# Performance work log

Hardware: AMD Instinct MI355X
Metric: run time of the kernel (lower is better)

The kernel has to match this reference:

```python
import jax, jax.numpy as jnp
import numpy as np

D_MODEL = 2048
N_Q = 32
N_KV = 8
HEAD_DIM = D_MODEL // N_Q  # 64
N_REP = N_Q // N_KV        # 4
QKV_OUT = HEAD_DIM * (N_Q + 2 * N_KV)  # 3072


def setup_inputs() -> dict:
    key = jax.random.key(0)
    ks = jax.random.split(key, 6)
    s = 1.0 / np.sqrt(D_MODEL)
    x = jax.random.normal(ks[0], (2, 2048, D_MODEL), dtype=jnp.float32)
    Wqkv = jax.random.normal(ks[1], (D_MODEL, QKV_OUT), dtype=jnp.float32) * s
    bqkv = jax.random.normal(ks[2], (QKV_OUT,), dtype=jnp.float32) * 0.02
    Wo = jax.random.normal(ks[3], (D_MODEL, D_MODEL), dtype=jnp.float32) * s
    bo = jax.random.normal(ks[4], (D_MODEL,), dtype=jnp.float32) * 0.02
    return {"x": x, "Wqkv": Wqkv, "bqkv": bqkv, "Wo": Wo, "bo": bo}


def reference(x, Wqkv, bqkv, Wo, bo):
    bsz, seqlen, _ = x.shape
    qkv = jnp.einsum('bsd,df->bsf', x, Wqkv) + bqkv
    q_end = HEAD_DIM * N_Q
    k_end = q_end + HEAD_DIM * N_KV
    q = qkv[..., :q_end].reshape(bsz, seqlen, N_Q, HEAD_DIM)
    k = qkv[..., q_end:k_end].reshape(bsz, seqlen, N_KV, HEAD_DIM)
    v = qkv[..., k_end:].reshape(bsz, seqlen, N_KV, HEAD_DIM)
    # GQA expansion: repeat kv heads n_rep times -> [b, s, N_Q, hd]
    k = jnp.repeat(k, N_REP, axis=2)
    v = jnp.repeat(v, N_REP, axis=2)
    # scores [b, h, s, s]
    scores = jnp.einsum('bqhd,bkhd->bhqk', q, k) / np.sqrt(HEAD_DIM).astype(np.float32)
    attn = jax.nn.softmax(scores, axis=-1)
    out = jnp.einsum('bhqk,bkhd->bqhd', attn, v).reshape(bsz, seqlen, D_MODEL)
    return jnp.einsum('bsd,de->bse', out, Wo) + bo
```

## Files before the change

kernel.cpp:

```cpp
#include <hip/hip_runtime.h>
#include <stdint.h>

typedef __attribute__((ext_vector_type(8))) __bf16 bf16x8;
typedef __attribute__((ext_vector_type(4))) float f32x4;
typedef uint16_t u16;
typedef __attribute__((address_space(1))) uint32_t ga_u32;
typedef __attribute__((address_space(3))) uint32_t lds_u32;

#define MFMA16(a, b, c) __builtin_amdgcn_mfma_f32_16x16x32_bf16(a, b, c, 0, 0, 0)

static __device__ __forceinline__ u16 f2bf(float f) {
  uint32_t u = __float_as_uint(f);
  u += 0x7FFFu + ((u >> 16) & 1u);
  return (u16)(u >> 16);
}

static __device__ __forceinline__ void async_cp16(const void* src, void* dst) {
  __builtin_amdgcn_global_load_lds((ga_u32*)src, (lds_u32*)dst, 16, 0, 0);
}

__global__ void cast_bf16_kernel(const float* __restrict__ in, u16* __restrict__ out, int n4) {
  int i = blockIdx.x * 256 + threadIdx.x;
  if (i < n4) {
    float4 v = reinterpret_cast<const float4*>(in)[i];
    ushort4 o;
    o.x = f2bf(v.x); o.y = f2bf(v.y); o.z = f2bf(v.z); o.w = f2bf(v.w);
    reinterpret_cast<ushort4*>(out)[i] = o;
  }
}

__global__ void transpose_cast_kernel(const float* __restrict__ W, u16* __restrict__ WT,
                                      int K, int N) {
  __shared__ float tile[32][33];
  int tx = threadIdx.x & 31, ty = threadIdx.x >> 5;
  int n0 = blockIdx.x * 32, k0 = blockIdx.y * 32;
#pragma unroll
  for (int i = 0; i < 32; i += 8)
    tile[ty + i][tx] = W[(size_t)(k0 + ty + i) * N + n0 + tx];
  __syncthreads();
#pragma unroll
  for (int i = 0; i < 32; i += 8)
    WT[(size_t)(n0 + ty + i) * K + k0 + tx] = f2bf(tile[tx][ty + i]);
}

template <int MODE>
__global__ void gemm_bt_kernel(const u16* __restrict__ A, const u16* __restrict__ BT,
                               const float* __restrict__ bias, void* __restrict__ C,
                               u16* __restrict__ vT,
                               int NBX, int N, int K, int OUTN) {
  __shared__ __align__(16) u16 sA[2][128 * 32];
  __shared__ __align__(16) u16 sB[2][128 * 32];
  int tid = threadIdx.x, lane = tid & 63, wave = tid >> 6;
  int wm = wave >> 1, wn = wave & 1;
  int nwg = gridDim.x, wid = blockIdx.x;
  int swz = (wid & 7) * (nwg >> 3) + (wid >> 3);
  int by = swz / NBX, bx = swz - by * NBX;
  int row0 = by * 128, col0 = bx * 128;
  int l15 = lane & 15, l4 = lane >> 4;

  int srow = wave * 32 + (lane >> 2);
  int sslot = (((lane & 3) ^ ((srow >> 1) & 3))) * 8;
  auto stage = [&](const u16* g, int r0, int k0, u16* lds) {
#pragma unroll
    for (int j = 0; j < 2; ++j) {
      const u16* src = g + (size_t)(r0 + srow + j * 16) * K + k0 + sslot;
      async_cp16(src, lds + (wave * 2 + j) * 512);
    }
  };

  f32x4 acc[4][4] = {};
  stage(A, row0, 0, sA[0]);
  stage(BT, col0, 0, sB[0]);
  __syncthreads();
  int nk = K >> 5, cur = 0;
  for (int kt = 0; kt < nk; ++kt) {
    if (kt + 1 < nk) {
      stage(A, row0, (kt + 1) * 32, sA[cur ^ 1]);
      stage(BT, col0, (kt + 1) * 32, sB[cur ^ 1]);
    }
    bf16x8 af[4], bfr[4];
#pragma unroll
    for (int m = 0; m < 4; ++m) {
      int ra = wm * 64 + m * 16 + l15;
      af[m] = *reinterpret_cast<const bf16x8*>(&sA[cur][ra * 32 + ((l4 ^ ((ra >> 1) & 3)) & 3) * 8]);
    }
#pragma unroll
    for (int n = 0; n < 4; ++n) {
      int rb = wn * 64 + n * 16 + l15;
      bfr[n] = *reinterpret_cast<const bf16x8*>(&sB[cur][rb * 32 + ((l4 ^ ((rb >> 1) & 3)) & 3) * 8]);
    }
#pragma unroll
    for (int m = 0; m < 4; ++m)
#pragma unroll
      for (int n = 0; n < 4; ++n)
        acc[m][n] = MFMA16(af[m], bfr[n], acc[m][n]);
    __syncthreads();
    cur ^= 1;
  }

  bool vpart = (MODE == 1) && (col0 >= 2560);
#pragma unroll
  for (int m = 0; m < 4; ++m) {
#pragma unroll
    for (int n = 0; n < 4; ++n) {
      int col = col0 + wn * 64 + n * 16 + l15;
      float bv = bias[col];
      int rowb = row0 + wm * 64 + m * 16 + l4 * 4;
      if (vpart) {
        int hk = (col - 2560) >> 6, d = col & 63;
        int b = rowb >> 11, s = rowb & 2047;
        ushort4 o;
        o.x = f2bf(acc[m][n][0] + bv); o.y = f2bf(acc[m][n][1] + bv);
        o.z = f2bf(acc[m][n][2] + bv); o.w = f2bf(acc[m][n][3] + bv);
        *reinterpret_cast<ushort4*>(&vT[((size_t)((b * 8 + hk) * 64 + d)) * 2048 + s]) = o;
      } else {
#pragma unroll
        for (int e = 0; e < 4; ++e) {
          float v = acc[m][n][e] + bv;
          if (MODE == 1)
            ((u16*)C)[(size_t)(rowb + e) * OUTN + col] = f2bf(v);
          else
            ((float*)C)[(size_t)(rowb + e) * OUTN + col] = v;
        }
      }
    }
  }
}

__global__ __launch_bounds__(256, 4)
void attn_kernel(const u16* __restrict__ qkv, const u16* __restrict__ vTg,
                 u16* __restrict__ attno) {
  __shared__ __align__(16) u16 Kl[2][64 * 64];
  __shared__ __align__(16) u16 Vl[2][64 * 64];
  __shared__ __align__(16) u16 Pw[4][1024];

  int wid = blockIdx.x;
  int swz = (wid & 7) * 128 + (wid >> 3);
  int qt = swz & 15, bh = swz >> 4;
  int b = bh >> 5, h = bh & 31, g = h >> 2;
  int tid = threadIdx.x, lane = tid & 63, w = tid >> 6;
  int l15 = lane & 15, l4 = lane >> 4;
  size_t rowbase = (size_t)b * 2048;

  bf16x8 aq[2][2];
#pragma unroll
  for (int qf = 0; qf < 2; ++qf)
#pragma unroll
    for (int ks = 0; ks < 2; ++ks)
      aq[qf][ks] = *reinterpret_cast<const bf16x8*>(
          qkv + (rowbase + qt * 128 + w * 32 + qf * 16 + l15) * 2560 + h * 64 + ks * 32 + l4 * 8);

  int src_r = lane >> 3;
  int sslot = ((lane & 7) ^ src_r) * 8;
  const u16* Kg = qkv + rowbase * 2560 + 2048 + g * 64;
  const u16* Vg = vTg + ((size_t)((b * 8 + g) * 64)) * 2048;

  auto stageKV = [&](int kt, int buf) {
#pragma unroll
    for (int j = 0; j < 2; ++j) {
      int c = w * 2 + j;
      async_cp16(Kg + (size_t)(kt * 64 + c * 8 + src_r) * 2560 + sslot, &Kl[buf][c * 512]);
    }
#pragma unroll
    for (int j = 0; j < 2; ++j) {
      int c = w * 2 + j;
      async_cp16(Vg + (size_t)(c * 8 + src_r) * 2048 + kt * 64 + sslot, &Vl[buf][c * 512]);
    }
  };

  f32x4 oacc[2][4] = {};
  f32x4 lacc[2] = {};
  union { short s[8]; bf16x8 v; } ones;
#pragma unroll
  for (int i = 0; i < 8; ++i) ones.s[i] = 0x3F80;

  stageKV(0, 0);
  const float CEXP = 0.18033688011112042f;
  char* pwb = (char*)&Pw[w][0];

  for (int kt = 0; kt < 32; ++kt) {
    int cur = kt & 1;
    __syncthreads();
    if (kt + 1 < 32) stageKV(kt + 1, cur ^ 1);

    f32x4 s[2][4] = {};
#pragma unroll
    for (int ks = 0; ks < 2; ++ks) {
      bf16x8 bk[4];
#pragma unroll
      for (int kf = 0; kf < 4; ++kf) {
        int key = kf * 16 + l15;
        bk[kf] = *reinterpret_cast<const bf16x8*>(
            &Kl[cur][key * 64 + (((ks * 4 + l4) ^ (key & 7)) * 8)]);
      }
#pragma unroll
      for (int qf = 0; qf < 2; ++qf)
#pragma unroll
        for (int kf = 0; kf < 4; ++kf)
          s[qf][kf] = MFMA16(bk[kf], aq[qf][ks], s[qf][kf]);
    }

#pragma unroll
    for (int qf = 0; qf < 2; ++qf)
#pragma unroll
      for (int kf = 0; kf < 4; ++kf)
#pragma unroll
        for (int e = 0; e < 4; ++e)
          s[qf][kf][e] = __builtin_amdgcn_exp2f(s[qf][kf][e] * CEXP);

#pragma unroll
    for (int kc = 0; kc < 2; ++kc) {
#pragma unroll
      for (int qf = 0; qf < 2; ++qf) {
        int ql = qf * 16 + l15;
#pragma unroll
        for (int kh = 0; kh < 2; ++kh) {
          union { ushort4 u; __bf16 bb[4]; } pk;
#pragma unroll
          for (int e = 0; e < 4; ++e) pk.bb[e] = (__bf16)s[qf][kc * 2 + kh][e];
          int off = ((ql << 6) + (kh << 5) + (l4 << 3)) ^ ((ql & 3) << 4);
          *reinterpret_cast<ushort4*>(pwb + off) = pk.u;
        }
      }
      asm volatile("" ::: "memory");
      bf16x8 pa[2], bv[4];
#pragma unroll
      for (int qf = 0; qf < 2; ++qf) {
        int ql = qf * 16 + l15;
        int off = ((ql << 6) + (l4 << 4)) ^ ((ql & 3) << 4);
        pa[qf] = *reinterpret_cast<const bf16x8*>(pwb + off);
      }
#pragma unroll
      for (int df = 0; df < 4; ++df) {
        int d = df * 16 + l15;
        bv[df] = *reinterpret_cast<const bf16x8*>(
            &Vl[cur][d * 64 + (((kc * 4 + l4) ^ (d & 7)) * 8)]);
      }
#pragma unroll
      for (int qf = 0; qf < 2; ++qf) {
        lacc[qf] = MFMA16(pa[qf], ones.v, lacc[qf]);
#pragma unroll
        for (int df = 0; df < 4; ++df)
          oacc[qf][df] = MFMA16(pa[qf], bv[df], oacc[qf][df]);
      }
      asm volatile("" ::: "memory");
    }
  }

#pragma unroll
  for (int qf = 0; qf < 2; ++qf)
#pragma unroll
    for (int df = 0; df < 4; ++df) {
      int col = h * 64 + df * 16 + l15;
#pragma unroll
      for (int e = 0; e < 4; ++e) {
        size_t row = rowbase + qt * 128 + w * 32 + qf * 16 + l4 * 4 + e;
        attno[row * 2048 + col] = f2bf(oacc[qf][df][e] / lacc[qf][e]);
      }
    }
}

extern "C" void kernel_launch(void* const* d_in, const int* in_sizes, int n_in,
                              void* d_out, int out_size, void* d_ws, size_t ws_size,
                              hipStream_t stream) {
  const float* x    = (const float*)d_in[0];
  const float* Wqkv = (const float*)d_in[1];
  const float* bqkv = (const float*)d_in[2];
  const float* Wo   = (const float*)d_in[3];
  const float* bo   = (const float*)d_in[4];
  float* out = (float*)d_out;

  char* ws = (char*)d_ws;
  u16* x_bf   = (u16*)(ws);
  u16* WqkvT  = (u16*)(ws + 16777216);
  u16* WoT    = (u16*)(ws + 29360128);
  u16* qkv_bf = (u16*)(ws + 37748736);
  u16* attno  = (u16*)(ws + 58720256);
  u16* vT     = (u16*)(ws + 75497472);

  cast_bf16_kernel<<<8192, 256, 0, stream>>>(x, x_bf, 2097152);
  transpose_cast_kernel<<<dim3(96, 64), 256, 0, stream>>>(Wqkv, WqkvT, 2048, 3072);
  transpose_cast_kernel<<<dim3(64, 64), 256, 0, stream>>>(Wo, WoT, 2048, 2048);
  gemm_bt_kernel<1><<<768, 256, 0, stream>>>(x_bf, WqkvT, bqkv, qkv_bf, vT,
                                             24, 3072, 2048, 2560);
  attn_kernel<<<1024, 256, 0, stream>>>(qkv_bf, vT, attno);
  gemm_bt_kernel<0><<<512, 256, 0, stream>>>(attno, WoT, bo, out, nullptr,
                                             16, 2048, 2048, 2048);
}
```

Measured before the change: 314.9 us.

## Enlarge GEMM and attention tiles to raise K/V and B-tile reuse

The GEMM kernel now runs 512 threads per block with a 256x128 tile, so eight waves share each staged B tile and the grid halves. The attention kernel gives each wave 64 query rows instead of 32, reusing each staged K/V tile across twice as many queries. It also computes the full 64-key score block per query fragment before the PV pass, with a larger per-wave P buffer and a wider XOR swizzle. The trade is more registers and LDS per block, lower occupancy (launch bounds lowered to 2), and fewer blocks to fill the GPU.

```diff
diff --git a/kernel.cpp b/kernel.cpp
--- a/kernel.cpp
+++ b/kernel.cpp
@@ -44,40 +44,40 @@
 }
 
 template <int MODE>
-__global__ void gemm_bt_kernel(const u16* __restrict__ A, const u16* __restrict__ BT,
-                               const float* __restrict__ bias, void* __restrict__ C,
-                               u16* __restrict__ vT,
-                               int NBX, int N, int K, int OUTN) {
-  __shared__ __align__(16) u16 sA[2][128 * 32];
+__global__ __launch_bounds__(512)
+void gemm_bt_kernel(const u16* __restrict__ A, const u16* __restrict__ BT,
+                    const float* __restrict__ bias, void* __restrict__ C,
+                    u16* __restrict__ vT,
+                    int NBX, int N, int K, int OUTN) {
+  __shared__ __align__(16) u16 sA[2][256 * 32];
   __shared__ __align__(16) u16 sB[2][128 * 32];
   int tid = threadIdx.x, lane = tid & 63, wave = tid >> 6;
   int wm = wave >> 1, wn = wave & 1;
   int nwg = gridDim.x, wid = blockIdx.x;
   int swz = (wid & 7) * (nwg >> 3) + (wid >> 3);
   int by = swz / NBX, bx = swz - by * NBX;
-  int row0 = by * 128, col0 = bx * 128;
+  int row0 = by * 256, col0 = bx * 128;
   int l15 = lane & 15, l4 = lane >> 4;
 
-  int srow = wave * 32 + (lane >> 2);
-  int sslot = (((lane & 3) ^ ((srow >> 1) & 3))) * 8;
-  auto stage = [&](const u16* g, int r0, int k0, u16* lds) {
-#pragma unroll
-    for (int j = 0; j < 2; ++j) {
-      const u16* src = g + (size_t)(r0 + srow + j * 16) * K + k0 + sslot;
-      async_cp16(src, lds + (wave * 2 + j) * 512);
-    }
+  int srowA = wave * 32 + (lane >> 2);
+  int sslotA = (((lane & 3) ^ ((srowA >> 1) & 3))) * 8;
+  int srowB = wave * 16 + (lane >> 2);
+  int sslotB = (((lane & 3) ^ ((srowB >> 1) & 3))) * 8;
+
+  auto stage = [&](int k0, int buf) {
+#pragma unroll
+    for (int j = 0; j < 2; ++j)
+      async_cp16(A + (size_t)(row0 + srowA + j * 16) * K + k0 + sslotA,
+                 &sA[buf][(wave * 2 + j) * 512]);
+    async_cp16(BT + (size_t)(col0 + srowB) * K + k0 + sslotB, &sB[buf][wave * 512]);
   };
 
   f32x4 acc[4][4] = {};
-  stage(A, row0, 0, sA[0]);
-  stage(BT, col0, 0, sB[0]);
+  stage(0, 0);
   __syncthreads();
   int nk = K >> 5, cur = 0;
   for (int kt = 0; kt < nk; ++kt) {
-    if (kt + 1 < nk) {
-      stage(A, row0, (kt + 1) * 32, sA[cur ^ 1]);
-      stage(BT, col0, (kt + 1) * 32, sB[cur ^ 1]);
-    }
+    if (kt + 1 < nk) stage((kt + 1) * 32, cur ^ 1);
     bf16x8 af[4], bfr[4];
 #pragma unroll
     for (int m = 0; m < 4; ++m) {
@@ -127,28 +127,28 @@
   }
 }
 
-__global__ __launch_bounds__(256, 4)
+__global__ __launch_bounds__(256, 2)
 void attn_kernel(const u16* __restrict__ qkv, const u16* __restrict__ vTg,
                  u16* __restrict__ attno) {
   __shared__ __align__(16) u16 Kl[2][64 * 64];
   __shared__ __align__(16) u16 Vl[2][64 * 64];
-  __shared__ __align__(16) u16 Pw[4][1024];
+  __shared__ __align__(16) u16 Pw[4][64 * 64];
 
   int wid = blockIdx.x;
-  int swz = (wid & 7) * 128 + (wid >> 3);
-  int qt = swz & 15, bh = swz >> 4;
+  int swz = (wid & 7) * 64 + (wid >> 3);
+  int qt = swz & 7, bh = swz >> 3;
   int b = bh >> 5, h = bh & 31, g = h >> 2;
   int tid = threadIdx.x, lane = tid & 63, w = tid >> 6;
   int l15 = lane & 15, l4 = lane >> 4;
   size_t rowbase = (size_t)b * 2048;
 
-  bf16x8 aq[2][2];
-#pragma unroll
-  for (int qf = 0; qf < 2; ++qf)
+  bf16x8 aq[4][2];
+#pragma unroll
+  for (int qf = 0; qf < 4; ++qf)
 #pragma unroll
     for (int ks = 0; ks < 2; ++ks)
       aq[qf][ks] = *reinterpret_cast<const bf16x8*>(
-          qkv + (rowbase + qt * 128 + w * 32 + qf * 16 + l15) * 2560 + h * 64 + ks * 32 + l4 * 8);
+          qkv + (rowbase + qt * 256 + w * 64 + qf * 16 + l15) * 2560 + h * 64 + ks * 32 + l4 * 8);
 
   int src_r = lane >> 3;
   int sslot = ((lane & 7) ^ src_r) * 8;
@@ -168,8 +168,8 @@
     }
   };
 
-  f32x4 oacc[2][4] = {};
-  f32x4 lacc[2] = {};
+  f32x4 oacc[4][4] = {};
+  f32x4 lacc[4] = {};
   union { short s[8]; bf16x8 v; } ones;
 #pragma unroll
   for (int i = 0; i < 8; ++i) ones.s[i] = 0x3F80;
@@ -183,53 +183,39 @@
     __syncthreads();
     if (kt + 1 < 32) stageKV(kt + 1, cur ^ 1);
 
-    f32x4 s[2][4] = {};
-#pragma unroll
-    for (int ks = 0; ks < 2; ++ks) {
-      bf16x8 bk[4];
+    bf16x8 bk[2][4];
+#pragma unroll
+    for (int ks = 0; ks < 2; ++ks)
 #pragma unroll
       for (int kf = 0; kf < 4; ++kf) {
         int key = kf * 16 + l15;
-        bk[kf] = *reinterpret_cast<const bf16x8*>(
+        bk[ks][kf] = *reinterpret_cast<const bf16x8*>(
             &Kl[cur][key * 64 + (((ks * 4 + l4) ^ (key & 7)) * 8)]);
       }
-#pragma unroll
-      for (int qf = 0; qf < 2; ++qf)
+
+#pragma unroll
+    for (int qf = 0; qf < 4; ++qf) {
+      f32x4 sq[4] = {};
+#pragma unroll
+      for (int ks = 0; ks < 2; ++ks)
 #pragma unroll
         for (int kf = 0; kf < 4; ++kf)
-          s[qf][kf] = MFMA16(bk[kf], aq[qf][ks], s[qf][kf]);
-    }
-
-#pragma unroll
-    for (int qf = 0; qf < 2; ++qf)
-#pragma unroll
-      for (int kf = 0; kf < 4; ++kf)
+          sq[kf] = MFMA16(bk[ks][kf], aq[qf][ks], sq[kf]);
+      int ql = qf * 16 + l15, rswz = (ql & 7) << 4;
+#pragma unroll
+      for (int kf = 0; kf < 4; ++kf) {
+        union { ushort4 u; __bf16 bb[4]; } pk;
 #pragma unroll
         for (int e = 0; e < 4; ++e)
-          s[qf][kf][e] = __builtin_amdgcn_exp2f(s[qf][kf][e] * CEXP);
+          pk.bb[e] = (__bf16)__builtin_amdgcn_exp2f(sq[kf][e] * CEXP);
+        *reinterpret_cast<ushort4*>(pwb + ((ql * 128 + kf * 32 + l4 * 8) ^ rswz)) = pk.u;
+      }
+    }
+    asm volatile("" ::: "memory");
 
 #pragma unroll
     for (int kc = 0; kc < 2; ++kc) {
-#pragma unroll
-      for (int qf = 0; qf < 2; ++qf) {
-        int ql = qf * 16 + l15;
-#pragma unroll
-        for (int kh = 0; kh < 2; ++kh) {
-          union { ushort4 u; __bf16 bb[4]; } pk;
-#pragma unroll
-          for (int e = 0; e < 4; ++e) pk.bb[e] = (__bf16)s[qf][kc * 2 + kh][e];
-          int off = ((ql << 6) + (kh << 5) + (l4 << 3)) ^ ((ql & 3) << 4);
-          *reinterpret_cast<ushort4*>(pwb + off) = pk.u;
-        }
-      }
-      asm volatile("" ::: "memory");
-      bf16x8 pa[2], bv[4];
-#pragma unroll
-      for (int qf = 0; qf < 2; ++qf) {
-        int ql = qf * 16 + l15;
-        int off = ((ql << 6) + (l4 << 4)) ^ ((ql & 3) << 4);
-        pa[qf] = *reinterpret_cast<const bf16x8*>(pwb + off);
-      }
+      bf16x8 bv[4];
 #pragma unroll
       for (int df = 0; df < 4; ++df) {
         int d = df * 16 + l15;
@@ -237,24 +223,26 @@
             &Vl[cur][d * 64 + (((kc * 4 + l4) ^ (d & 7)) * 8)]);
       }
 #pragma unroll
-      for (int qf = 0; qf < 2; ++qf) {
-        lacc[qf] = MFMA16(pa[qf], ones.v, lacc[qf]);
+      for (int qf = 0; qf < 4; ++qf) {
+        int ql = qf * 16 + l15;
+        bf16x8 pa = *reinterpret_cast<const bf16x8*>(
+            pwb + ((ql * 128 + kc * 64 + l4 * 16) ^ ((ql & 7) << 4)));
+        lacc[qf] = MFMA16(pa, ones.v, lacc[qf]);
 #pragma unroll
         for (int df = 0; df < 4; ++df)
-          oacc[qf][df] = MFMA16(pa[qf], bv[df], oacc[qf][df]);
-      }
-      asm volatile("" ::: "memory");
-    }
-  }
-
-#pragma unroll
-  for (int qf = 0; qf < 2; ++qf)
+          oacc[qf][df] = MFMA16(pa, bv[df], oacc[qf][df]);
+      }
+    }
+  }
+
+#pragma unroll
+  for (int qf = 0; qf < 4; ++qf)
 #pragma unroll
     for (int df = 0; df < 4; ++df) {
       int col = h * 64 + df * 16 + l15;
 #pragma unroll
       for (int e = 0; e < 4; ++e) {
-        size_t row = rowbase + qt * 128 + w * 32 + qf * 16 + l4 * 4 + e;
+        size_t row = rowbase + qt * 256 + w * 64 + qf * 16 + l4 * 4 + e;
         attno[row * 2048 + col] = f2bf(oacc[qf][df][e] / lacc[qf][e]);
       }
     }
@@ -281,9 +269,9 @@
   cast_bf16_kernel<<<8192, 256, 0, stream>>>(x, x_bf, 2097152);
   transpose_cast_kernel<<<dim3(96, 64), 256, 0, stream>>>(Wqkv, WqkvT, 2048, 3072);
   transpose_cast_kernel<<<dim3(64, 64), 256, 0, stream>>>(Wo, WoT, 2048, 2048);
-  gemm_bt_kernel<1><<<768, 256, 0, stream>>>(x_bf, WqkvT, bqkv, qkv_bf, vT,
+  gemm_bt_kernel<1><<<384, 512, 0, stream>>>(x_bf, WqkvT, bqkv, qkv_bf, vT,
                                              24, 3072, 2048, 2560);
-  attn_kernel<<<1024, 256, 0, stream>>>(qkv_bf, vT, attno);
-  gemm_bt_kernel<0><<<512, 256, 0, stream>>>(attno, WoT, bo, out, nullptr,
+  attn_kernel<<<512, 256, 0, stream>>>(qkv_bf, vT, attno);
+  gemm_bt_kernel<0><<<256, 512, 0, stream>>>(attno, WoT, bo, out, nullptr,
                                              16, 2048, 2048, 2048);
 }
```

Result: no change. 319.7 us (+1.5%).
